# Optimization experiments

Hardware: AMD Instinct MI355X
Metric: run time of the kernel (lower is better)

The kernel has to match this reference:

```python
import jax, jax.numpy as jnp
import numpy as np


def gcn_layer(x, W, b, src, dst):
    """PyG GCNConv with improved=True: A_hat = A + 2I, D^-1/2 A_hat D^-1/2 X W + b."""
    n = x.shape[0]
    xw = x @ W  # [N, H]
    # degree counts each incoming edge (weight 1) plus self-loop weight 2
    deg = jnp.zeros((n,), x.dtype).at[dst].add(jnp.ones((src.shape[0],), x.dtype)) + 2.0
    dinv = jax.lax.rsqrt(deg)  # deg >= 2 always
    norm = (dinv[src] * dinv[dst])[:, None]  # [E, 1]
    agg = jax.ops.segment_sum(xw[src] * norm, dst, num_segments=n)  # scatter-add to dst
    agg = agg + (2.0 * dinv * dinv)[:, None] * xw  # self-loop contribution (weight 2)
    return agg + b


def xavier(k, shape):
    lim = (6.0 / (shape[0] + shape[1])) ** 0.5
    return jax.random.uniform(k, shape, jnp.float32, -lim, lim)


def setup_inputs() -> dict:
    key = jax.random.key(0)
    ks = jax.random.split(key, 8)
    N, E, D = 100_000, 1_600_000, 64  # nodes, edges, features_dim
    H1, H2 = 64, 64                   # gnn_dims
    M1, M2 = 128, 64                  # ind_pol_dims
    rep = jax.random.normal(ks[0], (N, D), jnp.float32)
    edge_index = jax.random.randint(ks[1], (2, E), 0, N, jnp.int32)
    return {
        "rep": rep,
        "edge_index": edge_index,
        "W1": xavier(ks[2], (D, H1)), "b1": jnp.zeros((H1,), jnp.float32),
        "W2": xavier(ks[3], (H1, H2)), "b2": jnp.zeros((H2,), jnp.float32),
        "Wa": xavier(ks[4], (H2 + D, M1)), "ba": jnp.zeros((M1,), jnp.float32),
        "Wb": xavier(ks[5], (M1, M2)), "bb": jnp.zeros((M2,), jnp.float32),
        "Wo": xavier(ks[6], (M2, 1)), "bo": jnp.zeros((1,), jnp.float32),
    }


def reference(rep, edge_index, W1, b1, W2, b2, Wa, ba, Wb, bb, Wo, bo):
    src, dst = edge_index[0], edge_index[1]
    # eval mode: f.dropout(training=False) is identity
    h = jax.nn.relu(gcn_layer(rep, W1, b1, src, dst))
    h = jax.nn.relu(gcn_layer(h, W2, b2, src, dst))
    z = jnp.concatenate([rep, h], axis=1)  # [N, D + H2]
    z = jax.nn.relu(z @ Wa + ba)
    z = jax.nn.relu(z @ Wb + bb)
    prob = jax.nn.sigmoid(z @ Wo + bo)[:, 0]  # [N]
    # gumbel_softmax(hard=True, tau=1) over logits = [1-p, p] (torch semantics:
    # probabilities fed directly as logits, as in the original code)
    logits = jnp.stack([1.0 - prob, prob], axis=1)  # [N, 2]
    u = jax.random.uniform(jax.random.key(42), logits.shape, jnp.float32, 1e-20, 1.0)
    g = -jnp.log(-jnp.log(u))
    y = jax.nn.softmax(logits + g, axis=1)
    hard = jax.nn.one_hot(jnp.argmax(y, axis=1), 2, dtype=y.dtype)
    st = hard + y - jax.lax.stop_gradient(y)  # straight-through
    ind = st @ jnp.array([[0.0], [1.0]], dtype=y.dtype)  # mm with [[0],[1]]
    return (prob, ind[:, 0])
```

## Files before the change

kernel.cpp:

```cpp
#include <hip/hip_runtime.h>
#include <math.h>


__device__ __forceinline__ unsigned rotl32(unsigned x, int r) {
  return (x << r) | (x >> (32 - r));
}

__device__ __forceinline__ void threefry2x32(unsigned k0, unsigned k1,
                                             unsigned x0, unsigned x1,
                                             unsigned& o0, unsigned& o1) {
  unsigned ks2 = k0 ^ k1 ^ 0x1BD11BDAu;
#define TF_RND(r) { x0 += x1; x1 = rotl32(x1, (r)); x1 ^= x0; }
  x0 += k0; x1 += k1;
  TF_RND(13) TF_RND(15) TF_RND(26) TF_RND(6)
  x0 += k1; x1 += ks2 + 1u;
  TF_RND(17) TF_RND(29) TF_RND(16) TF_RND(24)
  x0 += ks2; x1 += k0 + 2u;
  TF_RND(13) TF_RND(15) TF_RND(26) TF_RND(6)
  x0 += k0; x1 += k1 + 3u;
  TF_RND(17) TF_RND(29) TF_RND(16) TF_RND(24)
  x0 += k1; x1 += ks2 + 4u;
  TF_RND(13) TF_RND(15) TF_RND(26) TF_RND(6)
  x0 += ks2; x1 += k0 + 5u;
#undef TF_RND
  o0 = x0; o1 = x1;
}

__device__ __forceinline__ unsigned jax_random_bits_u32(unsigned k0, unsigned k1,
                                                        unsigned flat_idx) {
  unsigned a, b;
  threefry2x32(k0, k1, 0u, flat_idx, a, b);
  return a ^ b;
}

#define BSHIFT 8
#define BMASK 255

__global__ __launch_bounds__(256) void coarse_hist_kernel(
    const int* __restrict__ dst, int* __restrict__ coarse, int E) {
  __shared__ int h[512];
  for (int i = threadIdx.x; i < 512; i += 256) h[i] = 0;
  __syncthreads();
  for (int e = blockIdx.x * blockDim.x + threadIdx.x; e < E;
       e += gridDim.x * blockDim.x)
    atomicAdd(&h[dst[e] >> BSHIFT], 1);
  __syncthreads();
  for (int i = threadIdx.x; i < 512; i += 256)
    if (h[i]) atomicAdd(&coarse[i], h[i]);
}

__global__ __launch_bounds__(512) void coarse_scan_kernel(
    const int* __restrict__ coarse, int* __restrict__ bbase,
    int* __restrict__ cbase, int NBUCK) {
  __shared__ int sh[512];
  int t = threadIdx.x;
  int v = (t < NBUCK) ? coarse[t] : 0;
  sh[t] = v;
  __syncthreads();
  for (int o = 1; o < 512; o <<= 1) {
    int a = (t >= o) ? sh[t - o] : 0;
    __syncthreads();
    sh[t] += a;
    __syncthreads();
  }
  if (t < NBUCK) {
    int ex = sh[t] - v;
    bbase[t] = ex;
    cbase[t] = ex;
    if (t == NBUCK - 1) bbase[NBUCK] = sh[t];
  }
}

#define CHUNK 4096
__global__ __launch_bounds__(256) void scatter_gemm_kernel(
    const int* __restrict__ src, const int* __restrict__ dst,
    int* __restrict__ cbase, int* __restrict__ pkB, int E, int nbA,
    const float* __restrict__ X, const float* __restrict__ W,
    float* __restrict__ Y, int N) {
  __shared__ int smem[9216];
  const int t = threadIdx.x;

  if (blockIdx.x < nbA) {
    int* sS = smem;
    int* dS = smem + 4096;
    int* cnt = smem + 8192;
    int* base = smem + 8704;
    const int e0 = blockIdx.x * CHUNK;
    const int n = min(CHUNK, E - e0);
    for (int i = t; i < 512; i += 256) cnt[i] = 0;
    for (int i = t; i < n; i += 256) {
      sS[i] = src[e0 + i];
      dS[i] = dst[e0 + i];
    }
    __syncthreads();
    for (int i = t; i < n; i += 256) atomicAdd(&cnt[dS[i] >> BSHIFT], 1);
    __syncthreads();
    for (int i = t; i < 512; i += 256) {
      int c = cnt[i];
      base[i] = c ? atomicAdd(&cbase[i], c) : 0;
    }
    __syncthreads();
    for (int i = t; i < 512; i += 256) cnt[i] = 0;
    __syncthreads();
    for (int i = t; i < n; i += 256) {
      int d = dS[i];
      int b = d >> BSHIFT;
      int r = atomicAdd(&cnt[b], 1);
      pkB[base[b] + r] = ((d & BMASK) << 20) | sS[i];
    }
    return;
  }

  float* Ws = (float*)smem;
  float* Xs = (float*)smem + 4096;
  {
    const float4* W4 = (const float4*)W;
    float4* Ws4 = (float4*)Ws;
    for (int i = t; i < 1024; i += 256) Ws4[i] = W4[i];
  }
  const int row0 = (blockIdx.x - nbA) * 64;
  for (int i = t; i < 64 * 16; i += 256) {
    int r = i >> 4, c4 = i & 15;
    int gr = row0 + r;
    float4 v = make_float4(0.f, 0.f, 0.f, 0.f);
    if (gr < N) v = *(const float4*)&X[(size_t)gr * 64 + c4 * 4];
    *(float4*)&Xs[r * 68 + c4 * 4] = v;
  }
  __syncthreads();

  const int tx = t & 15, ty = t >> 4;
  const int c0 = tx * 4;
  const int r0 = ty * 4;
  float acc[4][4];
#pragma unroll
  for (int i = 0; i < 4; ++i)
#pragma unroll
    for (int j = 0; j < 4; ++j) acc[i][j] = 0.f;

#pragma unroll 4
  for (int k4 = 0; k4 < 16; ++k4) {
    float4 xv[4];
#pragma unroll
    for (int i = 0; i < 4; ++i)
      xv[i] = *(const float4*)&Xs[(r0 + i) * 68 + k4 * 4];
#pragma unroll
    for (int kk = 0; kk < 4; ++kk) {
      float w[4];
#pragma unroll
      for (int j = 0; j < 4; ++j) w[j] = Ws[(k4 * 4 + kk) * 64 + c0 + j];
      const float xk[4] = {
          kk == 0 ? xv[0].x : kk == 1 ? xv[0].y : kk == 2 ? xv[0].z : xv[0].w,
          kk == 0 ? xv[1].x : kk == 1 ? xv[1].y : kk == 2 ? xv[1].z : xv[1].w,
          kk == 0 ? xv[2].x : kk == 1 ? xv[2].y : kk == 2 ? xv[2].z : xv[2].w,
          kk == 0 ? xv[3].x : kk == 1 ? xv[3].y : kk == 2 ? xv[3].z : xv[3].w};
#pragma unroll
      for (int i = 0; i < 4; ++i)
#pragma unroll
        for (int j = 0; j < 4; ++j) acc[i][j] = fmaf(xk[i], w[j], acc[i][j]);
    }
  }

#pragma unroll
  for (int i = 0; i < 4; ++i) {
    int gr = row0 + r0 + i;
    if (gr >= N) continue;
    float4 v = make_float4(acc[i][0], acc[i][1], acc[i][2], acc[i][3]);
    *(float4*)&Y[(size_t)gr * 64 + c0] = v;
  }
}

__global__ __launch_bounds__(256) void bucket_finalize_kernel(
    const int* __restrict__ pkB, const int* __restrict__ bbase,
    int* __restrict__ off, float* __restrict__ dinv, int* __restrict__ srcS,
    int N) {
  __shared__ int cnt[256];
  __shared__ int sh[256];
  const int t = threadIdx.x;
  const int b = blockIdx.x;
  const int lo = bbase[b], hi = bbase[b + 1];
  cnt[t] = 0;
  __syncthreads();
  for (int i = lo + t; i < hi; i += 256) atomicAdd(&cnt[pkB[i] >> 20], 1);
  __syncthreads();
  const int deg = cnt[t];
  sh[t] = deg;
  __syncthreads();
  for (int o = 1; o < 256; o <<= 1) {
    int a = (t >= o) ? sh[t - o] : 0;
    __syncthreads();
    sh[t] += a;
    __syncthreads();
  }
  const int ex = sh[t] - deg;
  const int node = (b << BSHIFT) + t;
  if (node < N) {
    off[node] = lo + ex;
    dinv[node] = 1.0f / sqrtf((float)deg + 2.0f);
    if (node == N - 1) off[N] = hi;
  }
  cnt[t] = lo + ex;
  __syncthreads();
  for (int i = lo + t; i < hi; i += 256) {
    int u = pkB[i];
    int pos = atomicAdd(&cnt[u >> 20], 1);
    srcS[pos] = u & 0xFFFFF;
  }
}

#define NPW 8
__global__ __launch_bounds__(256) void aggregate_kernel(
    const float* __restrict__ xws, const int* __restrict__ srcS,
    const int* __restrict__ off, const float* __restrict__ dinv,
    const float* __restrict__ dinvS, const float* __restrict__ bias,
    float* __restrict__ h, int N) {
  const int wid = (blockIdx.x * blockDim.x + threadIdx.x) >> 6;
  const int lane = threadIdx.x & 63;
  const int g = lane >> 4;
  const int fq = lane & 15;
  int node = wid * NPW;
  if (node >= N) return;
  const int nodeEnd = min(node + NPW, N);
  const float4* xw4 = (const float4*)xws;
  const float4 bq = ((const float4*)bias)[fq];
  int beg = off[node];
  for (; node < nodeEnd; ++node) {
    const int end = off[node + 1];
    float4 a0 = make_float4(0.f, 0.f, 0.f, 0.f);
    float4 a1 = a0, a2 = a0, a3 = a0;
    if (dinvS) {
      for (int e = beg; e < end; e += 16) {
        int e0 = e + g, e1 = e + 4 + g, e2 = e + 8 + g, e3 = e + 12 + g;
        int s0 = srcS[min(e0, end - 1)];
        int s1 = srcS[min(e1, end - 1)];
        int s2 = srcS[min(e2, end - 1)];
        int s3 = srcS[min(e3, end - 1)];
        float d0 = dinvS[s0], d1 = dinvS[s1], d2 = dinvS[s2], d3 = dinvS[s3];
        float4 v0 = xw4[(size_t)s0 * 16 + fq];
        float4 v1 = xw4[(size_t)s1 * 16 + fq];
        float4 v2 = xw4[(size_t)s2 * 16 + fq];
        float4 v3 = xw4[(size_t)s3 * 16 + fq];
        if (e0 < end) { a0.x += d0*v0.x; a0.y += d0*v0.y; a0.z += d0*v0.z; a0.w += d0*v0.w; }
        if (e1 < end) { a1.x += d1*v1.x; a1.y += d1*v1.y; a1.z += d1*v1.z; a1.w += d1*v1.w; }
        if (e2 < end) { a2.x += d2*v2.x; a2.y += d2*v2.y; a2.z += d2*v2.z; a2.w += d2*v2.w; }
        if (e3 < end) { a3.x += d3*v3.x; a3.y += d3*v3.y; a3.z += d3*v3.z; a3.w += d3*v3.w; }
      }
    } else {
      for (int e = beg; e < end; e += 16) {
        int e0 = e + g, e1 = e + 4 + g, e2 = e + 8 + g, e3 = e + 12 + g;
        int s0 = srcS[min(e0, end - 1)];
        int s1 = srcS[min(e1, end - 1)];
        int s2 = srcS[min(e2, end - 1)];
        int s3 = srcS[min(e3, end - 1)];
        float4 v0 = xw4[(size_t)s0 * 16 + fq];
        float4 v1 = xw4[(size_t)s1 * 16 + fq];
        float4 v2 = xw4[(size_t)s2 * 16 + fq];
        float4 v3 = xw4[(size_t)s3 * 16 + fq];
        if (e0 < end) { a0.x += v0.x; a0.y += v0.y; a0.z += v0.z; a0.w += v0.w; }
        if (e1 < end) { a1.x += v1.x; a1.y += v1.y; a1.z += v1.z; a1.w += v1.w; }
        if (e2 < end) { a2.x += v2.x; a2.y += v2.y; a2.z += v2.z; a2.w += v2.w; }
        if (e3 < end) { a3.x += v3.x; a3.y += v3.y; a3.z += v3.z; a3.w += v3.w; }
      }
    }
    float4 a;
    a.x = (a0.x + a1.x) + (a2.x + a3.x);
    a.y = (a0.y + a1.y) + (a2.y + a3.y);
    a.z = (a0.z + a1.z) + (a2.z + a3.z);
    a.w = (a0.w + a1.w) + (a2.w + a3.w);
    a.x += __shfl_xor(a.x, 16, 64); a.x += __shfl_xor(a.x, 32, 64);
    a.y += __shfl_xor(a.y, 16, 64); a.y += __shfl_xor(a.y, 32, 64);
    a.z += __shfl_xor(a.z, 16, 64); a.z += __shfl_xor(a.z, 32, 64);
    a.w += __shfl_xor(a.w, 16, 64); a.w += __shfl_xor(a.w, 32, 64);
    if (g == 0) {
      float di = dinv[node];
      float4 self = xw4[(size_t)node * 16 + fq];
      if (dinvS) { self.x *= di; self.y *= di; self.z *= di; self.w *= di; }
      float4 r;
      r.x = fmaxf(di * (a.x + 2.0f * self.x) + bq.x, 0.f);
      r.y = fmaxf(di * (a.y + 2.0f * self.y) + bq.y, 0.f);
      r.z = fmaxf(di * (a.z + 2.0f * self.z) + bq.z, 0.f);
      r.w = fmaxf(di * (a.w + 2.0f * self.w) + bq.w, 0.f);
      *(float4*)&h[(size_t)node * 64 + fq * 4] = r;
    }
    beg = end;
  }
}

__global__ __launch_bounds__(256) void gemm64v2_kernel(
    const float* __restrict__ X, const float* __restrict__ W,
    const float* __restrict__ dinv, float* __restrict__ Y, int N) {
  __shared__ float Ws[64 * 64];
  __shared__ float Xs[64 * 68];
  const int t = threadIdx.x;
  {
    const float4* W4 = (const float4*)W;
    float4* Ws4 = (float4*)Ws;
    for (int i = t; i < 16 * 64; i += 256) Ws4[i] = W4[i];
  }
  const int row0 = blockIdx.x * 64;
  for (int i = t; i < 64 * 16; i += 256) {
    int r = i >> 4, c4 = i & 15;
    int gr = row0 + r;
    float4 v = make_float4(0.f, 0.f, 0.f, 0.f);
    if (gr < N) v = *(const float4*)&X[(size_t)gr * 64 + c4 * 4];
    *(float4*)&Xs[r * 68 + c4 * 4] = v;
  }
  __syncthreads();

  const int tx = t & 15, ty = t >> 4;
  const int c0 = tx * 4;
  const int r0 = ty * 4;
  float acc[4][4];
#pragma unroll
  for (int i = 0; i < 4; ++i)
#pragma unroll
    for (int j = 0; j < 4; ++j) acc[i][j] = 0.f;

#pragma unroll 4
  for (int k4 = 0; k4 < 16; ++k4) {
    float4 xv[4];
#pragma unroll
    for (int i = 0; i < 4; ++i)
      xv[i] = *(const float4*)&Xs[(r0 + i) * 68 + k4 * 4];
#pragma unroll
    for (int kk = 0; kk < 4; ++kk) {
      float w[4];
#pragma unroll
      for (int j = 0; j < 4; ++j) w[j] = Ws[(k4 * 4 + kk) * 64 + c0 + j];
      const float xk[4] = {
          kk == 0 ? xv[0].x : kk == 1 ? xv[0].y : kk == 2 ? xv[0].z : xv[0].w,
          kk == 0 ? xv[1].x : kk == 1 ? xv[1].y : kk == 2 ? xv[1].z : xv[1].w,
          kk == 0 ? xv[2].x : kk == 1 ? xv[2].y : kk == 2 ? xv[2].z : xv[2].w,
          kk == 0 ? xv[3].x : kk == 1 ? xv[3].y : kk == 2 ? xv[3].z : xv[3].w};
#pragma unroll
      for (int i = 0; i < 4; ++i)
#pragma unroll
        for (int j = 0; j < 4; ++j) acc[i][j] = fmaf(xk[i], w[j], acc[i][j]);
    }
  }

#pragma unroll
  for (int i = 0; i < 4; ++i) {
    int gr = row0 + r0 + i;
    if (gr >= N) continue;
    float sc = dinv[gr];
    float4 v = make_float4(acc[i][0] * sc, acc[i][1] * sc, acc[i][2] * sc,
                           acc[i][3] * sc);
    *(float4*)&Y[(size_t)gr * 64 + c0] = v;
  }
}

__global__ __launch_bounds__(256) void head_mega_kernel(
    const float* __restrict__ rep, const float* __restrict__ h2,
    const float* __restrict__ Wa, const float* __restrict__ ba,
    const float* __restrict__ Wb, const float* __restrict__ bb,
    const float* __restrict__ Wo, const float* __restrict__ bo,
    float* __restrict__ out, int N) {
  __shared__ float Xs[64 * 128];
  __shared__ float Wd[2][1024];
  const int t = threadIdx.x;
  const int row0 = blockIdx.x * 64;

  for (int i = t; i < 2048; i += 256) {
    int r = i >> 5, c4 = i & 31;
    int gr = row0 + r;
    float4 v = make_float4(0.f, 0.f, 0.f, 0.f);
    if (gr < N)
      v = (c4 < 16) ? *(const float4*)&rep[(size_t)gr * 64 + c4 * 4]
                    : *(const float4*)&h2[(size_t)gr * 64 + (c4 - 16) * 4];
    int scol = (c4 * 4 + ((r >> 2) << 2)) & 127;
    *(float4*)&Xs[r * 128 + scol] = v;
  }

  const int tx = t & 15, ty = t >> 4;
  const int cL = tx * 4;
  const int cH = 64 + tx * 4;
  const int r0 = ty * 4;
  float za[4][8];
#pragma unroll
  for (int i = 0; i < 4; ++i)
#pragma unroll
    for (int j = 0; j < 8; ++j) za[i][j] = 0.f;

  const float4* Wa4 = (const float4*)Wa;
  {
    float4 w0 = Wa4[t];
    *(float4*)&Wd[0][t * 4] = w0;
  }
  __syncthreads();
  for (int c = 0; c < 16; ++c) {
    float4 wnext;
    if (c + 1 < 16) wnext = Wa4[(c + 1) * 256 + t];
    const float* Wcur = Wd[c & 1];
    const int kb = c * 8;
#pragma unroll
    for (int q = 0; q < 2; ++q) {
      const int kc0 = (kb + q * 4 + (ty << 2)) & 127;
      float4 xq[4];
#pragma unroll
      for (int i = 0; i < 4; ++i)
        xq[i] = *(const float4*)&Xs[(r0 + i) * 128 + kc0];
#pragma unroll
      for (int kk2 = 0; kk2 < 4; ++kk2) {
        const int kk = q * 4 + kk2;
        const float x[4] = {
            kk2 == 0 ? xq[0].x : kk2 == 1 ? xq[0].y : kk2 == 2 ? xq[0].z : xq[0].w,
            kk2 == 0 ? xq[1].x : kk2 == 1 ? xq[1].y : kk2 == 2 ? xq[1].z : xq[1].w,
            kk2 == 0 ? xq[2].x : kk2 == 1 ? xq[2].y : kk2 == 2 ? xq[2].z : xq[2].w,
            kk2 == 0 ? xq[3].x : kk2 == 1 ? xq[3].y : kk2 == 2 ? xq[3].z : xq[3].w};
        float4 w0 = *(const float4*)&Wcur[kk * 128 + cL];
        float4 w1 = *(const float4*)&Wcur[kk * 128 + cH];
        const float w[8] = {w0.x, w0.y, w0.z, w0.w, w1.x, w1.y, w1.z, w1.w};
#pragma unroll
        for (int i = 0; i < 4; ++i)
#pragma unroll
          for (int j = 0; j < 8; ++j) za[i][j] = fmaf(x[i], w[j], za[i][j]);
      }
    }
    if (c + 1 < 16) *(float4*)&Wd[(c + 1) & 1][t * 4] = wnext;
    __syncthreads();
  }

#pragma unroll
  for (int i = 0; i < 4; ++i) {
#pragma unroll
    for (int j = 0; j < 4; ++j) {
      za[i][j] = fmaxf(za[i][j] + ba[cL + j], 0.f);
      za[i][4 + j] = fmaxf(za[i][4 + j] + ba[cH + j], 0.f);
    }
  }

  float* zaS = Xs;
  const float4* Wb4 = (const float4*)Wb;
  {
    float4 wb0 = Wb4[t];
    *(float4*)&Wd[0][t * 4] = wb0;
    int sL = (cL + (ty << 2)) & 127;
    int sH = (cH + (ty << 2)) & 127;
#pragma unroll
    for (int i = 0; i < 4; ++i) {
      *(float4*)&zaS[(r0 + i) * 128 + sL] =
          make_float4(za[i][0], za[i][1], za[i][2], za[i][3]);
      *(float4*)&zaS[(r0 + i) * 128 + sH] =
          make_float4(za[i][4], za[i][5], za[i][6], za[i][7]);
    }
  }
  __syncthreads();

  const int c0b = tx * 4;
  float zb[4][4];
#pragma unroll
  for (int i = 0; i < 4; ++i)
#pragma unroll
    for (int j = 0; j < 4; ++j) zb[i][j] = 0.f;

  for (int c = 0; c < 8; ++c) {
    float4 wnext;
    if (c + 1 < 8) wnext = Wb4[(c + 1) * 256 + t];
    const float* Wcur = Wd[c & 1];
    const int kb = c * 16;
#pragma unroll
    for (int q = 0; q < 4; ++q) {
      const int kc0 = (kb + q * 4 + (ty << 2)) & 127;
      float4 xq[4];
#pragma unroll
      for (int i = 0; i < 4; ++i)
        xq[i] = *(const float4*)&zaS[(r0 + i) * 128 + kc0];
#pragma unroll
      for (int kk2 = 0; kk2 < 4; ++kk2) {
        const int kk = q * 4 + kk2;
        const float x[4] = {
            kk2 == 0 ? xq[0].x : kk2 == 1 ? xq[0].y : kk2 == 2 ? xq[0].z : xq[0].w,
            kk2 == 0 ? xq[1].x : kk2 == 1 ? xq[1].y : kk2 == 2 ? xq[1].z : xq[1].w,
            kk2 == 0 ? xq[2].x : kk2 == 1 ? xq[2].y : kk2 == 2 ? xq[2].z : xq[2].w,
            kk2 == 0 ? xq[3].x : kk2 == 1 ? xq[3].y : kk2 == 2 ? xq[3].z : xq[3].w};
        float4 w = *(const float4*)&Wcur[kk * 64 + c0b];
        const float wj[4] = {w.x, w.y, w.z, w.w};
#pragma unroll
        for (int i = 0; i < 4; ++i)
#pragma unroll
          for (int j = 0; j < 4; ++j) zb[i][j] = fmaf(x[i], wj[j], zb[i][j]);
      }
    }
    if (c + 1 < 8) *(float4*)&Wd[(c + 1) & 1][t * 4] = wnext;
    __syncthreads();
  }

  float part[4];
#pragma unroll
  for (int i = 0; i < 4; ++i) {
    part[i] = 0.f;
#pragma unroll
    for (int j = 0; j < 4; ++j) {
      float v = fmaxf(zb[i][j] + bb[c0b + j], 0.f);
      part[i] = fmaf(v, Wo[c0b + j], part[i]);
    }
  }
  float* red = Xs;
#pragma unroll
  for (int i = 0; i < 4; ++i) red[tx * 68 + r0 + i] = part[i];
  __syncthreads();
  if (t < 64) {
    int gr = row0 + t;
    if (gr < N) {
      float s = 0.f;
#pragma unroll
      for (int u = 0; u < 16; ++u) s += red[u * 68 + t];
      float w = s + bo[0];
      float p = 1.0f / (1.0f + expf(-w));
      unsigned i = (unsigned)gr;
      unsigned bits0 = jax_random_bits_u32(0u, 42u, 2u * i);
      unsigned bits1 = jax_random_bits_u32(0u, 42u, 2u * i + 1u);
      float f0 = __uint_as_float((bits0 >> 9) | 0x3f800000u) - 1.0f;
      float f1 = __uint_as_float((bits1 >> 9) | 0x3f800000u) - 1.0f;
      float u0 = fmaxf(1e-20f, f0 + 1e-20f);
      float u1 = fmaxf(1e-20f, f1 + 1e-20f);
      float g0 = -logf(-logf(u0));
      float g1 = -logf(-logf(u1));
      float a0 = (1.0f - p) + g0;
      float a1 = p + g1;
      float m = fmaxf(a0, a1);
      float e0 = expf(a0 - m), e1 = expf(a1 - m);
      float ssum = e0 + e1;
      float y0 = e0 / ssum, y1 = e1 / ssum;
      float hard1 = (y1 > y0) ? 1.0f : 0.0f;
      float st1 = (hard1 + y1) - y1;
      out[gr] = p;
      out[N + gr] = st1;
    }
  }
}

extern "C" void kernel_launch(void* const* d_in, const int* in_sizes, int n_in,
                              void* d_out, int out_size, void* d_ws, size_t ws_size,
                              hipStream_t stream) {
  const float* rep = (const float*)d_in[0];
  const int* ei = (const int*)d_in[1];
  const float* W1 = (const float*)d_in[2];
  const float* b1 = (const float*)d_in[3];
  const float* W2 = (const float*)d_in[4];
  const float* b2 = (const float*)d_in[5];
  const float* Wa = (const float*)d_in[6];
  const float* ba = (const float*)d_in[7];
  const float* Wb = (const float*)d_in[8];
  const float* bb = (const float*)d_in[9];
  const float* Wo = (const float*)d_in[10];
  const float* bo = (const float*)d_in[11];
  float* out = (float*)d_out;

  const int N = in_sizes[0] / 64;
  const int E = in_sizes[1] / 2;
  const int* srcI = ei;
  const int* dstI = ei + E;

  const int NBUCK = (N + 255) >> BSHIFT;

  float* ws = (float*)d_ws;
  float* bufA = ws;
  float* bufB = bufA + (size_t)N * 64;
  float* dinv = bufB + (size_t)N * 64;
  int* coarse = (int*)(dinv + N);
  int* bbase = coarse + 512;
  int* cbase = bbase + 513;
  int* off = cbase + 512;
  int* pkB = off + N + 1;
  int* srcS = pkB + E;

  const int nb64 = (N + 63) / 64;
  const int nbW = (N + 4 * NPW - 1) / (4 * NPW);
  const int nbA = (E + CHUNK - 1) / CHUNK;

  hipMemsetAsync(coarse, 0, 512 * 4, stream);
  coarse_hist_kernel<<<256, 256, 0, stream>>>(dstI, coarse, E);
  coarse_scan_kernel<<<1, 512, 0, stream>>>(coarse, bbase, cbase, NBUCK);
  scatter_gemm_kernel<<<nbA + nb64, 256, 0, stream>>>(
      srcI, dstI, cbase, pkB, E, nbA, rep, W1, bufA, N);
  bucket_finalize_kernel<<<NBUCK, 256, 0, stream>>>(pkB, bbase, off, dinv,
                                                    srcS, N);

  aggregate_kernel<<<nbW, 256, 0, stream>>>(bufA, srcS, off, dinv, dinv, b1,
                                            bufB, N);

  gemm64v2_kernel<<<nb64, 256, 0, stream>>>(bufB, W2, dinv, bufA, N);
  aggregate_kernel<<<nbW, 256, 0, stream>>>(bufA, srcS, off, dinv, nullptr, b2,
                                            bufB, N);

  head_mega_kernel<<<nb64, 256, 0, stream>>>(rep, bufB, Wa, ba, Wb, bb, Wo, bo,
                                             out, N);
}
```

Measured before the change: 383.3 us.

## Fuse neighbor aggregation into following GEMM and head MLP kernels

```diff
diff --git a/kernel.cpp b/kernel.cpp
--- a/kernel.cpp
+++ b/kernel.cpp
@@ -207,102 +207,97 @@
   }
 }
 
-#define NPW 8
-__global__ __launch_bounds__(256) void aggregate_kernel(
-    const float* __restrict__ xws, const int* __restrict__ srcS,
+__device__ __forceinline__ float4 agg_edges(
+    const float4* __restrict__ xw4, const int* __restrict__ srcS,
+    int beg, int end, const float* __restrict__ dinvS, int g, int fq) {
+  float4 a0 = make_float4(0.f, 0.f, 0.f, 0.f);
+  float4 a1 = a0, a2 = a0, a3 = a0;
+  if (dinvS) {
+    for (int e = beg; e < end; e += 16) {
+      int e0 = e + g, e1 = e + 4 + g, e2 = e + 8 + g, e3 = e + 12 + g;
+      int s0 = srcS[min(e0, end - 1)];
+      int s1 = srcS[min(e1, end - 1)];
+      int s2 = srcS[min(e2, end - 1)];
+      int s3 = srcS[min(e3, end - 1)];
+      float d0 = dinvS[s0], d1 = dinvS[s1], d2 = dinvS[s2], d3 = dinvS[s3];
+      float4 v0 = xw4[(size_t)s0 * 16 + fq];
+      float4 v1 = xw4[(size_t)s1 * 16 + fq];
+      float4 v2 = xw4[(size_t)s2 * 16 + fq];
+      float4 v3 = xw4[(size_t)s3 * 16 + fq];
+      if (e0 < end) { a0.x += d0*v0.x; a0.y += d0*v0.y; a0.z += d0*v0.z; a0.w += d0*v0.w; }
+      if (e1 < end) { a1.x += d1*v1.x; a1.y += d1*v1.y; a1.z += d1*v1.z; a1.w += d1*v1.w; }
+      if (e2 < end) { a2.x += d2*v2.x; a2.y += d2*v2.y; a2.z += d2*v2.z; a2.w += d2*v2.w; }
+      if (e3 < end) { a3.x += d3*v3.x; a3.y += d3*v3.y; a3.z += d3*v3.z; a3.w += d3*v3.w; }
+    }
+  } else {
+    for (int e = beg; e < end; e += 16) {
+      int e0 = e + g, e1 = e + 4 + g, e2 = e + 8 + g, e3 = e + 12 + g;
+      int s0 = srcS[min(e0, end - 1)];
+      int s1 = srcS[min(e1, end - 1)];
+      int s2 = srcS[min(e2, end - 1)];
+      int s3 = srcS[min(e3, end - 1)];
+      float4 v0 = xw4[(size_t)s0 * 16 + fq];
+      float4 v1 = xw4[(size_t)s1 * 16 + fq];
+      float4 v2 = xw4[(size_t)s2 * 16 + fq];
+      float4 v3 = xw4[(size_t)s3 * 16 + fq];
+      if (e0 < end) { a0.x += v0.x; a0.y += v0.y; a0.z += v0.z; a0.w += v0.w; }
+      if (e1 < end) { a1.x += v1.x; a1.y += v1.y; a1.z += v1.z; a1.w += v1.w; }
+      if (e2 < end) { a2.x += v2.x; a2.y += v2.y; a2.z += v2.z; a2.w += v2.w; }
+      if (e3 < end) { a3.x += v3.x; a3.y += v3.y; a3.z += v3.z; a3.w += v3.w; }
+    }
+  }
+  float4 a;
+  a.x = (a0.x + a1.x) + (a2.x + a3.x);
+  a.y = (a0.y + a1.y) + (a2.y + a3.y);
+  a.z = (a0.z + a1.z) + (a2.z + a3.z);
+  a.w = (a0.w + a1.w) + (a2.w + a3.w);
+  a.x += __shfl_xor(a.x, 16, 64); a.x += __shfl_xor(a.x, 32, 64);
+  a.y += __shfl_xor(a.y, 16, 64); a.y += __shfl_xor(a.y, 32, 64);
+  a.z += __shfl_xor(a.z, 16, 64); a.z += __shfl_xor(a.z, 32, 64);
+  a.w += __shfl_xor(a.w, 16, 64); a.w += __shfl_xor(a.w, 32, 64);
+  return a;
+}
+
+__global__ __launch_bounds__(256) void agg1_gemm2_kernel(
+    const float* __restrict__ xw1, const int* __restrict__ srcS,
     const int* __restrict__ off, const float* __restrict__ dinv,
-    const float* __restrict__ dinvS, const float* __restrict__ bias,
-    float* __restrict__ h, int N) {
-  const int wid = (blockIdx.x * blockDim.x + threadIdx.x) >> 6;
-  const int lane = threadIdx.x & 63;
-  const int g = lane >> 4;
-  const int fq = lane & 15;
-  int node = wid * NPW;
-  if (node >= N) return;
-  const int nodeEnd = min(node + NPW, N);
-  const float4* xw4 = (const float4*)xws;
-  const float4 bq = ((const float4*)bias)[fq];
-  int beg = off[node];
-  for (; node < nodeEnd; ++node) {
-    const int end = off[node + 1];
-    float4 a0 = make_float4(0.f, 0.f, 0.f, 0.f);
-    float4 a1 = a0, a2 = a0, a3 = a0;
-    if (dinvS) {
-      for (int e = beg; e < end; e += 16) {
-        int e0 = e + g, e1 = e + 4 + g, e2 = e + 8 + g, e3 = e + 12 + g;
-        int s0 = srcS[min(e0, end - 1)];
-        int s1 = srcS[min(e1, end - 1)];
-        int s2 = srcS[min(e2, end - 1)];
-        int s3 = srcS[min(e3, end - 1)];
-        float d0 = dinvS[s0], d1 = dinvS[s1], d2 = dinvS[s2], d3 = dinvS[s3];
-        float4 v0 = xw4[(size_t)s0 * 16 + fq];
-        float4 v1 = xw4[(size_t)s1 * 16 + fq];
-        float4 v2 = xw4[(size_t)s2 * 16 + fq];
-        float4 v3 = xw4[(size_t)s3 * 16 + fq];
-        if (e0 < end) { a0.x += d0*v0.x; a0.y += d0*v0.y; a0.z += d0*v0.z; a0.w += d0*v0.w; }
-        if (e1 < end) { a1.x += d1*v1.x; a1.y += d1*v1.y; a1.z += d1*v1.z; a1.w += d1*v1.w; }
-        if (e2 < end) { a2.x += d2*v2.x; a2.y += d2*v2.y; a2.z += d2*v2.z; a2.w += d2*v2.w; }
-        if (e3 < end) { a3.x += d3*v3.x; a3.y += d3*v3.y; a3.z += d3*v3.z; a3.w += d3*v3.w; }
+    const float* __restrict__ b1, const float* __restrict__ W2,
+    float* __restrict__ Y, int N) {
+  __shared__ float Hs[64 * 68];
+  __shared__ float Ws[64 * 64];
+  const int t = threadIdx.x;
+  const int row0 = blockIdx.x * 64;
+  const int lane = t & 63, lw = t >> 6;
+  const int g = lane >> 4, fq = lane & 15;
+
+  {
+    const float4* W4 = (const float4*)W2;
+    float4* Ws4 = (float4*)Ws;
+    for (int i = t; i < 1024; i += 256) Ws4[i] = W4[i];
+  }
+
+  const float4* xw4 = (const float4*)xw1;
+  const float4 bq = ((const float4*)b1)[fq];
+  const int node0 = row0 + lw * 16;
+  const int nodeEnd = min(node0 + 16, N);
+  if (node0 < N) {
+    int beg = off[node0];
+    for (int node = node0; node < nodeEnd; ++node) {
+      const int end = off[node + 1];
+      float4 a = agg_edges(xw4, srcS, beg, end, dinv, g, fq);
+      if (g == 0) {
+        float di = dinv[node];
+        float4 self = xw4[(size_t)node * 16 + fq];
+        self.x *= di; self.y *= di; self.z *= di; self.w *= di;
+        float4 r;
+        r.x = fmaxf(di * (a.x + 2.0f * self.x) + bq.x, 0.f);
+        r.y = fmaxf(di * (a.y + 2.0f * self.y) + bq.y, 0.f);
+        r.z = fmaxf(di * (a.z + 2.0f * self.z) + bq.z, 0.f);
+        r.w = fmaxf(di * (a.w + 2.0f * self.w) + bq.w, 0.f);
+        *(float4*)&Hs[(node - row0) * 68 + fq * 4] = r;
       }
-    } else {
-      for (int e = beg; e < end; e += 16) {
-        int e0 = e + g, e1 = e + 4 + g, e2 = e + 8 + g, e3 = e + 12 + g;
-        int s0 = srcS[min(e0, end - 1)];
-        int s1 = srcS[min(e1, end - 1)];
-        int s2 = srcS[min(e2, end - 1)];
-        int s3 = srcS[min(e3, end - 1)];
-        float4 v0 = xw4[(size_t)s0 * 16 + fq];
-        float4 v1 = xw4[(size_t)s1 * 16 + fq];
-        float4 v2 = xw4[(size_t)s2 * 16 + fq];
-        float4 v3 = xw4[(size_t)s3 * 16 + fq];
-        if (e0 < end) { a0.x += v0.x; a0.y += v0.y; a0.z += v0.z; a0.w += v0.w; }
-        if (e1 < end) { a1.x += v1.x; a1.y += v1.y; a1.z += v1.z; a1.w += v1.w; }
-        if (e2 < end) { a2.x += v2.x; a2.y += v2.y; a2.z += v2.z; a2.w += v2.w; }
-        if (e3 < end) { a3.x += v3.x; a3.y += v3.y; a3.z += v3.z; a3.w += v3.w; }
-      }
-    }
-    float4 a;
-    a.x = (a0.x + a1.x) + (a2.x + a3.x);
-    a.y = (a0.y + a1.y) + (a2.y + a3.y);
-    a.z = (a0.z + a1.z) + (a2.z + a3.z);
-    a.w = (a0.w + a1.w) + (a2.w + a3.w);
-    a.x += __shfl_xor(a.x, 16, 64); a.x += __shfl_xor(a.x, 32, 64);
-    a.y += __shfl_xor(a.y, 16, 64); a.y += __shfl_xor(a.y, 32, 64);
-    a.z += __shfl_xor(a.z, 16, 64); a.z += __shfl_xor(a.z, 32, 64);
-    a.w += __shfl_xor(a.w, 16, 64); a.w += __shfl_xor(a.w, 32, 64);
-    if (g == 0) {
-      float di = dinv[node];
-      float4 self = xw4[(size_t)node * 16 + fq];
-      if (dinvS) { self.x *= di; self.y *= di; self.z *= di; self.w *= di; }
-      float4 r;
-      r.x = fmaxf(di * (a.x + 2.0f * self.x) + bq.x, 0.f);
-      r.y = fmaxf(di * (a.y + 2.0f * self.y) + bq.y, 0.f);
-      r.z = fmaxf(di * (a.z + 2.0f * self.z) + bq.z, 0.f);
-      r.w = fmaxf(di * (a.w + 2.0f * self.w) + bq.w, 0.f);
-      *(float4*)&h[(size_t)node * 64 + fq * 4] = r;
-    }
-    beg = end;
-  }
-}
-
-__global__ __launch_bounds__(256) void gemm64v2_kernel(
-    const float* __restrict__ X, const float* __restrict__ W,
-    const float* __restrict__ dinv, float* __restrict__ Y, int N) {
-  __shared__ float Ws[64 * 64];
-  __shared__ float Xs[64 * 68];
-  const int t = threadIdx.x;
-  {
-    const float4* W4 = (const float4*)W;
-    float4* Ws4 = (float4*)Ws;
-    for (int i = t; i < 16 * 64; i += 256) Ws4[i] = W4[i];
-  }
-  const int row0 = blockIdx.x * 64;
-  for (int i = t; i < 64 * 16; i += 256) {
-    int r = i >> 4, c4 = i & 15;
-    int gr = row0 + r;
-    float4 v = make_float4(0.f, 0.f, 0.f, 0.f);
-    if (gr < N) v = *(const float4*)&X[(size_t)gr * 64 + c4 * 4];
-    *(float4*)&Xs[r * 68 + c4 * 4] = v;
+      beg = end;
+    }
   }
   __syncthreads();
 
@@ -320,7 +315,7 @@
     float4 xv[4];
 #pragma unroll
     for (int i = 0; i < 4; ++i)
-      xv[i] = *(const float4*)&Xs[(r0 + i) * 68 + k4 * 4];
+      xv[i] = *(const float4*)&Hs[(r0 + i) * 68 + k4 * 4];
 #pragma unroll
     for (int kk = 0; kk < 4; ++kk) {
       float w[4];
@@ -349,8 +344,10 @@
   }
 }
 
-__global__ __launch_bounds__(256) void head_mega_kernel(
-    const float* __restrict__ rep, const float* __restrict__ h2,
+__global__ __launch_bounds__(256) void agg2_head_kernel(
+    const float* __restrict__ xw2, const int* __restrict__ srcS,
+    const int* __restrict__ off, const float* __restrict__ dinv,
+    const float* __restrict__ b2, const float* __restrict__ rep,
     const float* __restrict__ Wa, const float* __restrict__ ba,
     const float* __restrict__ Wb, const float* __restrict__ bb,
     const float* __restrict__ Wo, const float* __restrict__ bo,
@@ -359,17 +356,54 @@
   __shared__ float Wd[2][1024];
   const int t = threadIdx.x;
   const int row0 = blockIdx.x * 64;
+  const int lane = t & 63, lw = t >> 6;
+  const int g = lane >> 4, fq = lane & 15;
 
   for (int i = t; i < 2048; i += 256) {
     int r = i >> 5, c4 = i & 31;
     int gr = row0 + r;
-    float4 v = make_float4(0.f, 0.f, 0.f, 0.f);
-    if (gr < N)
-      v = (c4 < 16) ? *(const float4*)&rep[(size_t)gr * 64 + c4 * 4]
-                    : *(const float4*)&h2[(size_t)gr * 64 + (c4 - 16) * 4];
     int scol = (c4 * 4 + ((r >> 2) << 2)) & 127;
-    *(float4*)&Xs[r * 128 + scol] = v;
-  }
+    if (c4 < 16) {
+      float4 v = make_float4(0.f, 0.f, 0.f, 0.f);
+      if (gr < N) v = *(const float4*)&rep[(size_t)gr * 64 + c4 * 4];
+      *(float4*)&Xs[r * 128 + scol] = v;
+    } else if (gr >= N) {
+      *(float4*)&Xs[r * 128 + scol] = make_float4(0.f, 0.f, 0.f, 0.f);
+    }
+  }
+  const float4* Wa4 = (const float4*)Wa;
+  {
+    float4 w0 = Wa4[t];
+    *(float4*)&Wd[0][t * 4] = w0;
+  }
+
+  {
+    const float4* xw4 = (const float4*)xw2;
+    const float4 bq = ((const float4*)b2)[fq];
+    const int node0 = row0 + lw * 16;
+    const int nodeEnd = min(node0 + 16, N);
+    if (node0 < N) {
+      int beg = off[node0];
+      for (int node = node0; node < nodeEnd; ++node) {
+        const int end = off[node + 1];
+        float4 a = agg_edges(xw4, srcS, beg, end, nullptr, g, fq);
+        if (g == 0) {
+          float di = dinv[node];
+          float4 self = xw4[(size_t)node * 16 + fq];
+          float4 r;
+          r.x = fmaxf(di * (a.x + 2.0f * self.x) + bq.x, 0.f);
+          r.y = fmaxf(di * (a.y + 2.0f * self.y) + bq.y, 0.f);
+          r.z = fmaxf(di * (a.z + 2.0f * self.z) + bq.z, 0.f);
+          r.w = fmaxf(di * (a.w + 2.0f * self.w) + bq.w, 0.f);
+          const int rr = node - row0;
+          const int scol = ((64 + fq * 4) + ((rr >> 2) << 2)) & 127;
+          *(float4*)&Xs[rr * 128 + scol] = r;
+        }
+        beg = end;
+      }
+    }
+  }
+  __syncthreads();
 
   const int tx = t & 15, ty = t >> 4;
   const int cL = tx * 4;
@@ -381,12 +415,6 @@
 #pragma unroll
     for (int j = 0; j < 8; ++j) za[i][j] = 0.f;
 
-  const float4* Wa4 = (const float4*)Wa;
-  {
-    float4 w0 = Wa4[t];
-    *(float4*)&Wd[0][t * 4] = w0;
-  }
-  __syncthreads();
   for (int c = 0; c < 16; ++c) {
     float4 wnext;
     if (c + 1 < 16) wnext = Wa4[(c + 1) * 256 + t];
@@ -566,7 +594,6 @@
   int* srcS = pkB + E;
 
   const int nb64 = (N + 63) / 64;
-  const int nbW = (N + 4 * NPW - 1) / (4 * NPW);
   const int nbA = (E + CHUNK - 1) / CHUNK;
 
   hipMemsetAsync(coarse, 0, 512 * 4, stream);
@@ -577,13 +604,9 @@
   bucket_finalize_kernel<<<NBUCK, 256, 0, stream>>>(pkB, bbase, off, dinv,
                                                     srcS, N);
 
-  aggregate_kernel<<<nbW, 256, 0, stream>>>(bufA, srcS, off, dinv, dinv, b1,
-                                            bufB, N);
-
-  gemm64v2_kernel<<<nb64, 256, 0, stream>>>(bufB, W2, dinv, bufA, N);
-  aggregate_kernel<<<nbW, 256, 0, stream>>>(bufA, srcS, off, dinv, nullptr, b2,
-                                            bufB, N);
-
-  head_mega_kernel<<<nb64, 256, 0, stream>>>(rep, bufB, Wa, ba, Wb, bb, Wo, bo,
-                                             out, N);
-}
+  agg1_gemm2_kernel<<<nb64, 256, 0, stream>>>(bufA, srcS, off, dinv, b1, W2,
+                                              bufB, N);
+
+  agg2_head_kernel<<<nb64, 256, 0, stream>>>(bufB, srcS, off, dinv, b2, rep,
+                                             Wa, ba, Wb, bb, Wo, bo, out, N);
+}
```

Measured after the change: 466.7 us. 21.7% more time.
